# Kernel optimization log

Hardware: AMD Instinct MI355X
Metric: run time of the kernel (lower is better)

The kernel has to match this reference:

```python
import jax, jax.numpy as jnp
import numpy as np

N = 300000   # nodes
E = 1500000  # edges
G = 30000    # graphs
R = 3        # relations
EMB = 32
HID = 64
OUT = 2


def rgcn_conv(x, src, dst, edge_type, W, root, bias, num_nodes):
    """PyG RGCNConv: out_i = x_i @ root + bias + sum_r mean_{j in N_r(i)} x_j @ W_r."""
    out = x @ root + bias
    for r in range(W.shape[0]):
        xr = x @ W[r]                                  # [N, out] transform once per relation
        mask = (edge_type == r).astype(x.dtype)        # [E]
        msg = xr[src] * mask[:, None]                  # gather + mask  [E, out]
        agg = jax.ops.segment_sum(msg, dst, num_segments=num_nodes)
        cnt = jax.ops.segment_sum(mask, dst, num_segments=num_nodes)
        out = out + agg / jnp.maximum(cnt, 1.0)[:, None]
    return out


def global_mean_pool(x, batch, num_graphs):
    s = jax.ops.segment_sum(x, batch, num_segments=num_graphs)
    c = jax.ops.segment_sum(jnp.ones((x.shape[0],), x.dtype), batch, num_segments=num_graphs)
    return s / jnp.maximum(c, 1.0)[:, None]


def setup_inputs() -> dict:
    key = jax.random.key(0)
    ks = jax.random.split(key, 16)
    def glorot(k, shape):
        fan_in, fan_out = shape[-2], shape[-1]
        lim = np.sqrt(6.0 / (fan_in + fan_out)).astype(np.float32)
        return jax.random.uniform(k, shape, jnp.float32, -lim, lim)
    return {
        "sid": jax.random.randint(ks[0], (N,), 0, 26),
        "cid": jax.random.randint(ks[1], (N,), 0, 10),
        "pid": jax.random.randint(ks[2], (N,), 0, 128),
        "edge_index": jax.random.randint(ks[3], (2, E), 0, N),
        "edge_type": jax.random.randint(ks[4], (E,), 0, R),
        "batch": jnp.sort(jax.random.randint(ks[5], (N,), 0, G)),
        "num_graphs": G,
        "shape_emb": jax.random.normal(ks[6], (26, EMB), jnp.float32),
        "col_emb": jax.random.normal(ks[7], (10, EMB), jnp.float32),
        "pos_emb": jax.random.normal(ks[8], (128, EMB), jnp.float32),
        "W1": glorot(ks[9], (R, EMB, HID)),
        "root1": glorot(ks[10], (EMB, HID)),
        "b1": jnp.zeros((HID,), jnp.float32),
        "W2": glorot(ks[11], (R, HID, HID)),
        "root2": glorot(ks[12], (HID, HID)),
        "b2": jnp.zeros((HID,), jnp.float32),
        "lin_W": glorot(ks[13], (HID, OUT)),
        "lin_b": jnp.zeros((OUT,), jnp.float32),
    }


def reference(sid, cid, pid, edge_index, edge_type, batch, num_graphs,
              shape_emb, col_emb, pos_emb,
              W1, root1, b1, W2, root2, b2, lin_W, lin_b):
    num_nodes = sid.shape[0]
    src, dst = edge_index[0], edge_index[1]
    x = shape_emb[sid] + col_emb[cid] + pos_emb[pid]          # [N, 32]
    x = jax.nn.relu(rgcn_conv(x, src, dst, edge_type, W1, root1, b1, num_nodes))
    x = jax.nn.relu(rgcn_conv(x, src, dst, edge_type, W2, root2, b2, num_nodes))
    g = global_mean_pool(x, batch, num_graphs)                 # [G, 64]
    return g @ lin_W + lin_b                                   # [G, 2]
```

## Files before the change

kernel.cpp:

```cpp
#include <hip/hip_runtime.h>
#include <hip/hip_bf16.h>

#define NREL 3
#define EMB 32
#define HID 64
#define OVCAP 1024
#define BCAP 1024

typedef __attribute__((ext_vector_type(8))) short short8_t;
typedef __attribute__((ext_vector_type(4))) short short4_t;
typedef __attribute__((ext_vector_type(4))) float f32x4;

__device__ inline short f2bf(float v) {
  __hip_bfloat16 b = __float2bfloat16(v);
  short s;
  __builtin_memcpy(&s, &b, 2);
  return s;
}
__device__ inline float bf2f(short s) {
  __hip_bfloat16 b;
  __builtin_memcpy(&b, &s, 2);
  return __bfloat162float(b);
}
__device__ inline void split8(const float* v, short8_t* h, short8_t* l) {
#pragma unroll
  for (int i = 0; i < 8; i++) {
    short hh = f2bf(v[i]);
    (*h)[i] = hh;
    (*l)[i] = f2bf(v[i] - bf2f(hh));
  }
}

__global__ __launch_bounds__(256) void prep_k(
    const int* __restrict__ sid, const int* __restrict__ cid, const int* __restrict__ pid,
    const float* __restrict__ se, const float* __restrict__ ce, const float* __restrict__ pe,
    short* __restrict__ xh, short* __restrict__ xl,
    const int* __restrict__ src, const int* __restrict__ dst, const int* __restrict__ et,
    int* __restrict__ bcur, unsigned* __restrict__ pk,
    const float* __restrict__ root1, const float* __restrict__ W1,
    const float* __restrict__ root2, const float* __restrict__ W2,
    short* __restrict__ w1h, short* __restrict__ w1l,
    short* __restrict__ w2h, short* __restrict__ w2l, int N, int E) {
  int i = blockIdx.x * 256 + threadIdx.x;
  if (i < N * 8) {
    int n = i >> 3, cg = i & 7;
    const float4 a = *(const float4*)&se[sid[n] * EMB + cg * 4];
    const float4 b = *(const float4*)&ce[cid[n] * EMB + cg * 4];
    const float4 c = *(const float4*)&pe[pid[n] * EMB + cg * 4];
    float v[4];
    v[0] = a.x + b.x + c.x; v[1] = a.y + b.y + c.y;
    v[2] = a.z + b.z + c.z; v[3] = a.w + b.w + c.w;
    short4_t h, l;
#pragma unroll
    for (int j = 0; j < 4; j++) {
      short hh = f2bf(v[j]);
      h[j] = hh;
      l[j] = f2bf(v[j] - bf2f(hh));
    }
    *(short4_t*)&xh[(size_t)n * EMB + cg * 4] = h;
    *(short4_t*)&xl[(size_t)n * EMB + cg * 4] = l;
  }
  if (i < E) {
    int d = dst[i];
    int b = d >> 6;
    int j = atomicAdd(&bcur[b * 16], 1);
    if (j < BCAP)
      pk[(size_t)b * BCAP + j] =
          ((unsigned)(d & 63) << 21) | ((unsigned)et[i] << 19) | (unsigned)src[i];
  }
  if (i < 64 * 128) {
    int k = i >> 6, n = i & 63;
    float v = (k < EMB) ? root1[k * 64 + n] : W1[(k - EMB) * 64 + n];
    short h = f2bf(v);
    w1h[n * 128 + k] = h;
    w1l[n * 128 + k] = f2bf(v - bf2f(h));
  }
  if (i < 64 * 256) {
    int k = i >> 6, n = i & 63;
    float v = (k < HID) ? root2[k * 64 + n] : W2[(k - HID) * 64 + n];
    short h = f2bf(v);
    w2h[n * 256 + k] = h;
    w2l[n * 256 + k] = f2bf(v - bf2f(h));
  }
}

__global__ __launch_bounds__(256) void l1fused_k(
    const short* __restrict__ xh, const short* __restrict__ xl,
    const int* __restrict__ bcur, const unsigned* __restrict__ pk,
    const short* __restrict__ wth, const short* __restrict__ wtl,
    const float* __restrict__ bias, short* __restrict__ h1h, short* __restrict__ h1l, int N) {
  __shared__ __align__(16) short lws[64][16][8];
  __shared__ __align__(16) int4 mid_s[192];
  __shared__ int cnt_s[192];
  __shared__ unsigned ovf_s[OVCAP];
  __shared__ int ovfn_s;

  const int t = threadIdx.x;
  const int lane = t & 63, w = t >> 6;
  const int m_ = lane & 15, q = lane >> 4;
  const int n0b = blockIdx.x * 64;

  int node_c = n0b + w * 16 + m_;
  if (node_c >= N) node_c = N - 1;
  short8_t ah0 = *(const short8_t*)&xh[(size_t)node_c * EMB + q * 8];
  short8_t al0 = *(const short8_t*)&xl[(size_t)node_c * EMB + q * 8];
#pragma unroll
  for (int i = 0; i < 4; i++) {
    int chi = t + 256 * i;
    int row = chi >> 4, c = chi & 15;
    short8_t wv = *(const short8_t*)&wth[(size_t)row * 128 + c * 8];
    *(short8_t*)&lws[row][c ^ (row & 7)][0] = wv;
  }
  if (t < 192) cnt_s[t] = 0;
  if (t == 0) ovfn_s = 0;
  __syncthreads();

  {
    int ne = bcur[blockIdx.x * 16];
    if (ne > BCAP) ne = BCAP;
    const size_t base = (size_t)blockIdx.x * BCAP;
    for (int e = t; e < ne; e += 256) {
      unsigned p = pk[base + e];
      int srcn = (int)(p & 0x7FFFF);
      int slot = (int)((p >> 19) & 3) * 64 + (int)(p >> 21);
      int j = atomicAdd(&cnt_s[slot], 1);
      if (j < 4) ((int*)&mid_s[slot])[j] = srcn;
      else {
        int k2 = atomicAdd(&ovfn_s, 1);
        if (k2 < OVCAP) ovf_s[k2] = ((unsigned)slot << 19) | (unsigned)srcn;
      }
    }
  }
  __syncthreads();

  short8_t ahv[4], alv[4];
  ahv[0] = ah0;
  alv[0] = al0;
  {
    int ovn = ovfn_s;
    if (ovn > OVCAP) ovn = OVCAP;
    int tslot[3], tlen[3];
    int4 tid4[3];
#pragma unroll
    for (int k = 0; k < 3; k++) {
      tslot[k] = k * 64 + w * 16 + m_;
      tid4[k] = mid_s[tslot[k]];
      tlen[k] = cnt_s[tslot[k]];
    }
    short8_t v0[3], v1[3], v2[3], v3[3];
#pragma unroll
    for (int k = 0; k < 3; k++) {
      int nself = n0b + (tslot[k] & 63);
      if (nself >= N) nself = N - 1;
      int g0 = (0 < tlen[k]) ? tid4[k].x : nself;
      int g1 = (1 < tlen[k]) ? tid4[k].y : nself;
      int g2 = (2 < tlen[k]) ? tid4[k].z : nself;
      int g3 = (3 < tlen[k]) ? tid4[k].w : nself;
      size_t co = (size_t)q * 8;
      v0[k] = *(const short8_t*)&xh[(size_t)g0 * EMB + co];
      v1[k] = *(const short8_t*)&xh[(size_t)g1 * EMB + co];
      v2[k] = *(const short8_t*)&xh[(size_t)g2 * EMB + co];
      v3[k] = *(const short8_t*)&xh[(size_t)g3 * EMB + co];
    }
#pragma unroll
    for (int k = 0; k < 3; k++) {
      float a[8];
      float k0 = (0 < tlen[k]) ? 1.f : 0.f;
      float k1 = (1 < tlen[k]) ? 1.f : 0.f;
      float k2 = (2 < tlen[k]) ? 1.f : 0.f;
      float k3 = (3 < tlen[k]) ? 1.f : 0.f;
#pragma unroll
      for (int i = 0; i < 8; i++)
        a[i] = k0 * bf2f(v0[k][i]) + k1 * bf2f(v1[k][i]) + k2 * bf2f(v2[k][i]) +
               k3 * bf2f(v3[k][i]);
      for (int k3_ = 0; k3_ < ovn; k3_++) {
        unsigned ov = ovf_s[k3_];
        if ((int)(ov >> 19) == tslot[k]) {
          short8_t u = *(const short8_t*)&xh[(size_t)(ov & 0x7FFFF) * EMB + q * 8];
#pragma unroll
          for (int i = 0; i < 8; i++) a[i] += bf2f(u[i]);
        }
      }
      float inv = 1.f / fmaxf((float)tlen[k], 1.f);
#pragma unroll
      for (int i = 0; i < 8; i++) a[i] *= inv;
      split8(a, &ahv[k + 1], &alv[k + 1]);
    }
  }

  f32x4 acc[4];
#pragma unroll
  for (int i = 0; i < 4; i++) acc[i] = (f32x4){0.f, 0.f, 0.f, 0.f};
#pragma unroll
  for (int g = 0; g < 4; g++) {
#pragma unroll
    for (int tt = 0; tt < 4; tt++) {
      int row = 16 * tt + m_;
      int cs = (g * 4 + q) ^ (row & 7);
      short8_t bh = *(const short8_t*)&lws[row][cs][0];
      acc[tt] = __builtin_amdgcn_mfma_f32_16x16x32_bf16(ahv[g], bh, acc[tt], 0, 0, 0);
      acc[tt] = __builtin_amdgcn_mfma_f32_16x16x32_bf16(alv[g], bh, acc[tt], 0, 0, 0);
    }
  }
  __syncthreads();

#pragma unroll
  for (int i = 0; i < 4; i++) {
    int chi = t + 256 * i;
    int row = chi >> 4, c = chi & 15;
    short8_t wv = *(const short8_t*)&wtl[(size_t)row * 128 + c * 8];
    *(short8_t*)&lws[row][c ^ (row & 7)][0] = wv;
  }
  __syncthreads();

#pragma unroll
  for (int g = 0; g < 4; g++) {
#pragma unroll
    for (int tt = 0; tt < 4; tt++) {
      int row = 16 * tt + m_;
      int cs = (g * 4 + q) ^ (row & 7);
      short8_t bl = *(const short8_t*)&lws[row][cs][0];
      acc[tt] = __builtin_amdgcn_mfma_f32_16x16x32_bf16(ahv[g], bl, acc[tt], 0, 0, 0);
    }
  }
#pragma unroll
  for (int tt = 0; tt < 4; tt++) {
    float bia = bias[16 * tt + m_];
#pragma unroll
    for (int reg = 0; reg < 4; reg++) {
      int node = n0b + w * 16 + q * 4 + reg;
      if (node < N) {
        float val = fmaxf(acc[tt][reg] + bia, 0.f);
        short hh = f2bf(val);
        h1h[(size_t)node * HID + 16 * tt + m_] = hh;
        h1l[(size_t)node * HID + 16 * tt + m_] = f2bf(val - bf2f(hh));
      }
    }
  }
}

__global__ __launch_bounds__(256) void l2fused_k(
    const short* __restrict__ h1h, const short* __restrict__ h1l,
    const int* __restrict__ bcur, const unsigned* __restrict__ pk,
    const short* __restrict__ wth, const short* __restrict__ wtl,
    const float* __restrict__ bias, const float* __restrict__ linW,
    const int* __restrict__ batch, float* __restrict__ gs, float* __restrict__ gc, int N) {
  __shared__ __align__(16) short lws[64][16][8];
  __shared__ __align__(16) int4 mid_s[192];
  __shared__ int cnt_s[192];
  __shared__ unsigned ovf_s[OVCAP];
  __shared__ int ovfn_s;

  const int t = threadIdx.x;
  const int lane = t & 63, w = t >> 6;
  const int m_ = lane & 15, q = lane >> 4;
  const int n0b = blockIdx.x * 64;

  int node_c = n0b + w * 16 + m_;
  if (node_c >= N) node_c = N - 1;
#pragma unroll
  for (int i = 0; i < 4; i++) {
    int chi = t + 256 * i;
    int row = chi >> 4, c = chi & 15;
    int g = c >> 2, qq = c & 3;
    short8_t wv = *(const short8_t*)&wth[(size_t)row * 256 + g * 64 + 0 * 32 + qq * 8];
    *(short8_t*)&lws[row][c ^ (row & 7)][0] = wv;
  }
  if (t < 192) cnt_s[t] = 0;
  if (t == 0) ovfn_s = 0;
  __syncthreads();

  {
    int ne = bcur[blockIdx.x * 16];
    if (ne > BCAP) ne = BCAP;
    const size_t base = (size_t)blockIdx.x * BCAP;
    for (int e = t; e < ne; e += 256) {
      unsigned p = pk[base + e];
      int srcn = (int)(p & 0x7FFFF);
      int slot = (int)((p >> 19) & 3) * 64 + (int)(p >> 21);
      int j = atomicAdd(&cnt_s[slot], 1);
      if (j < 4) ((int*)&mid_s[slot])[j] = srcn;
      else {
        int k2 = atomicAdd(&ovfn_s, 1);
        if (k2 < OVCAP) ovf_s[k2] = ((unsigned)slot << 19) | (unsigned)srcn;
      }
    }
  }
  __syncthreads();

  short8_t ahv0[4], alv0[4], ahv1[4], alv1[4];
  {
    ahv0[0] = *(const short8_t*)&h1h[(size_t)node_c * HID + q * 8];
    alv0[0] = *(const short8_t*)&h1l[(size_t)node_c * HID + q * 8];
    ahv1[0] = *(const short8_t*)&h1h[(size_t)node_c * HID + 32 + q * 8];
    alv1[0] = *(const short8_t*)&h1l[(size_t)node_c * HID + 32 + q * 8];
    int ovn = ovfn_s;
    if (ovn > OVCAP) ovn = OVCAP;
    int tslot[3], tlen[3];
    int4 tid4[3];
    int gid[3][4];
#pragma unroll
    for (int k = 0; k < 3; k++) {
      tslot[k] = k * 64 + w * 16 + m_;
      tid4[k] = mid_s[tslot[k]];
      tlen[k] = cnt_s[tslot[k]];
      int nself = n0b + (tslot[k] & 63);
      if (nself >= N) nself = N - 1;
      gid[k][0] = (0 < tlen[k]) ? tid4[k].x : nself;
      gid[k][1] = (1 < tlen[k]) ? tid4[k].y : nself;
      gid[k][2] = (2 < tlen[k]) ? tid4[k].z : nself;
      gid[k][3] = (3 < tlen[k]) ? tid4[k].w : nself;
    }
    float a0[3][8], a1[3][8];
    {
      short8_t v0[3], v1[3], v2[3], v3[3];
#pragma unroll
      for (int k = 0; k < 3; k++) {
        size_t co = (size_t)q * 8;
        v0[k] = *(const short8_t*)&h1h[(size_t)gid[k][0] * HID + co];
        v1[k] = *(const short8_t*)&h1h[(size_t)gid[k][1] * HID + co];
        v2[k] = *(const short8_t*)&h1h[(size_t)gid[k][2] * HID + co];
        v3[k] = *(const short8_t*)&h1h[(size_t)gid[k][3] * HID + co];
      }
#pragma unroll
      for (int k = 0; k < 3; k++) {
        float k0 = (0 < tlen[k]) ? 1.f : 0.f;
        float k1 = (1 < tlen[k]) ? 1.f : 0.f;
        float k2 = (2 < tlen[k]) ? 1.f : 0.f;
        float k3 = (3 < tlen[k]) ? 1.f : 0.f;
#pragma unroll
        for (int i = 0; i < 8; i++)
          a0[k][i] = k0 * bf2f(v0[k][i]) + k1 * bf2f(v1[k][i]) + k2 * bf2f(v2[k][i]) +
                     k3 * bf2f(v3[k][i]);
      }
    }
    {
      short8_t v0[3], v1[3], v2[3], v3[3];
#pragma unroll
      for (int k = 0; k < 3; k++) {
        size_t co = 32 + (size_t)q * 8;
        v0[k] = *(const short8_t*)&h1h[(size_t)gid[k][0] * HID + co];
        v1[k] = *(const short8_t*)&h1h[(size_t)gid[k][1] * HID + co];
        v2[k] = *(const short8_t*)&h1h[(size_t)gid[k][2] * HID + co];
        v3[k] = *(const short8_t*)&h1h[(size_t)gid[k][3] * HID + co];
      }
#pragma unroll
      for (int k = 0; k < 3; k++) {
        float k0 = (0 < tlen[k]) ? 1.f : 0.f;
        float k1 = (1 < tlen[k]) ? 1.f : 0.f;
        float k2 = (2 < tlen[k]) ? 1.f : 0.f;
        float k3 = (3 < tlen[k]) ? 1.f : 0.f;
#pragma unroll
        for (int i = 0; i < 8; i++)
          a1[k][i] = k0 * bf2f(v0[k][i]) + k1 * bf2f(v1[k][i]) + k2 * bf2f(v2[k][i]) +
                     k3 * bf2f(v3[k][i]);
      }
    }
#pragma unroll
    for (int k = 0; k < 3; k++) {
      for (int k3_ = 0; k3_ < ovn; k3_++) {
        unsigned ov = ovf_s[k3_];
        if ((int)(ov >> 19) == tslot[k]) {
          const short* p = &h1h[(size_t)(ov & 0x7FFFF) * HID];
          short8_t u0 = *(const short8_t*)&p[q * 8];
          short8_t u1 = *(const short8_t*)&p[32 + q * 8];
#pragma unroll
          for (int i = 0; i < 8; i++) {
            a0[k][i] += bf2f(u0[i]);
            a1[k][i] += bf2f(u1[i]);
          }
        }
      }
      float inv = 1.f / fmaxf((float)tlen[k], 1.f);
#pragma unroll
      for (int i = 0; i < 8; i++) {
        a0[k][i] *= inv;
        a1[k][i] *= inv;
      }
      split8(a0[k], &ahv0[k + 1], &alv0[k + 1]);
      split8(a1[k], &ahv1[k + 1], &alv1[k + 1]);
    }
  }

  f32x4 acc[4];
#pragma unroll
  for (int i = 0; i < 4; i++) acc[i] = (f32x4){0.f, 0.f, 0.f, 0.f};
#pragma unroll
  for (int s_ = 0; s_ < 2; s_++) {
    if (s_ == 1) {
#pragma unroll
      for (int i = 0; i < 4; i++) {
        int chi = t + 256 * i;
        int row = chi >> 4, c = chi & 15;
        int g = c >> 2, q2 = c & 3;
        short8_t wv = *(const short8_t*)&wth[(size_t)row * 256 + g * 64 + 32 + q2 * 8];
        *(short8_t*)&lws[row][c ^ (row & 7)][0] = wv;
      }
      __syncthreads();
    }
#pragma unroll
    for (int g = 0; g < 4; g++) {
      short8_t ah = (s_ == 0) ? ahv0[g] : ahv1[g];
      short8_t al = (s_ == 0) ? alv0[g] : alv1[g];
#pragma unroll
      for (int tt = 0; tt < 4; tt++) {
        int row = 16 * tt + m_;
        int cs = (g * 4 + q) ^ (row & 7);
        short8_t bh = *(const short8_t*)&lws[row][cs][0];
        acc[tt] = __builtin_amdgcn_mfma_f32_16x16x32_bf16(ah, bh, acc[tt], 0, 0, 0);
        acc[tt] = __builtin_amdgcn_mfma_f32_16x16x32_bf16(al, bh, acc[tt], 0, 0, 0);
      }
    }
    __syncthreads();
#pragma unroll
    for (int i = 0; i < 4; i++) {
      int chi = t + 256 * i;
      int row = chi >> 4, c = chi & 15;
      int g = c >> 2, q2 = c & 3;
      short8_t wv = *(const short8_t*)&wtl[(size_t)row * 256 + g * 64 + s_ * 32 + q2 * 8];
      *(short8_t*)&lws[row][c ^ (row & 7)][0] = wv;
    }
    __syncthreads();
#pragma unroll
    for (int g = 0; g < 4; g++) {
      short8_t ah = (s_ == 0) ? ahv0[g] : ahv1[g];
#pragma unroll
      for (int tt = 0; tt < 4; tt++) {
        int row = 16 * tt + m_;
        int cs = (g * 4 + q) ^ (row & 7);
        short8_t bl = *(const short8_t*)&lws[row][cs][0];
        acc[tt] = __builtin_amdgcn_mfma_f32_16x16x32_bf16(ah, bl, acc[tt], 0, 0, 0);
      }
    }
    if (s_ == 0) __syncthreads();
  }

  float bia[4], lw0[4], lw1[4];
#pragma unroll
  for (int tt = 0; tt < 4; tt++) {
    int col = 16 * tt + m_;
    bia[tt] = bias[col];
    lw0[tt] = linW[col * 2 + 0];
    lw1[tt] = linW[col * 2 + 1];
  }
#pragma unroll
  for (int reg = 0; reg < 4; reg++) {
    int node = n0b + w * 16 + q * 4 + reg;
    float p0 = 0.f, p1 = 0.f;
#pragma unroll
    for (int tt = 0; tt < 4; tt++) {
      float v = fmaxf(acc[tt][reg] + bia[tt], 0.f);
      p0 += v * lw0[tt];
      p1 += v * lw1[tt];
    }
#pragma unroll
    for (int o = 1; o < 16; o <<= 1) {
      p0 += __shfl_xor(p0, o, 64);
      p1 += __shfl_xor(p1, o, 64);
    }
    if (m_ == 0 && node < N) {
      int g = batch[node];
      atomicAdd(&gs[g * 2 + 0], p0);
      atomicAdd(&gs[g * 2 + 1], p1);
      atomicAdd(&gc[g], 1.0f);
    }
  }
}

__global__ __launch_bounds__(256) void final_k(const float* __restrict__ gs,
                                               const float* __restrict__ gc,
                                               const float* __restrict__ linb,
                                               float* __restrict__ out, int G) {
  int i = blockIdx.x * 256 + threadIdx.x;
  if (i >= G * 2) return;
  int g = i >> 1, o = i & 1;
  out[i] = gs[i] / fmaxf(gc[g], 1.0f) + linb[o];
}

extern "C" void kernel_launch(void* const* d_in, const int* in_sizes, int n_in,
                              void* d_out, int out_size, void* d_ws, size_t ws_size,
                              hipStream_t stream) {
  const int* sid = (const int*)d_in[0];
  const int* cid = (const int*)d_in[1];
  const int* pid = (const int*)d_in[2];
  const int* ei = (const int*)d_in[3];
  const int* et = (const int*)d_in[4];
  const int* batch = (const int*)d_in[5];
  const float* se = (const float*)d_in[7];
  const float* ce = (const float*)d_in[8];
  const float* pe = (const float*)d_in[9];
  const float* W1 = (const float*)d_in[10];
  const float* root1 = (const float*)d_in[11];
  const float* b1 = (const float*)d_in[12];
  const float* W2 = (const float*)d_in[13];
  const float* root2 = (const float*)d_in[14];
  const float* b2 = (const float*)d_in[15];
  const float* linW = (const float*)d_in[16];
  const float* linb = (const float*)d_in[17];
  float* out = (float*)d_out;

  const int N = in_sizes[0];
  const int E = in_sizes[4];
  const int G = out_size / 2;
  const int* src = ei;
  const int* dst = ei + E;
  const int NBk = (N + 63) / 64;
  const int NBa = (NBk + 15) & ~15;

  char* w = (char*)d_ws;
  short* h1h = (short*)w;  w += (size_t)N * HID * sizeof(short);
  short* h1l = (short*)w;  w += (size_t)N * HID * sizeof(short);
  short* xh = (short*)w;   w += (size_t)N * EMB * sizeof(short);
  short* xl = (short*)w;   w += (size_t)N * EMB * sizeof(short);
  float* gs = (float*)w;   w += (size_t)G * 2 * sizeof(float);
  float* gc = (float*)w;   w += (size_t)G * sizeof(float);
  int* bcur = (int*)w;     w += (size_t)NBa * 16 * sizeof(int);
  unsigned* pk = (unsigned*)w; w += (size_t)NBa * BCAP * sizeof(unsigned);
  short* w1h = (short*)w;  w += (size_t)64 * 128 * sizeof(short);
  short* w1l = (short*)w;  w += (size_t)64 * 128 * sizeof(short);
  short* w2h = (short*)w;  w += (size_t)64 * 256 * sizeof(short);
  short* w2l = (short*)w;  w += (size_t)64 * 256 * sizeof(short);
  if ((size_t)(w - (char*)d_ws) > ws_size) return;

  hipMemsetAsync(bcur, 0, (size_t)NBa * 16 * sizeof(int), stream);
  hipMemsetAsync(gs, 0, (size_t)G * 3 * sizeof(float), stream);

  int prep_n = N * 8;
  if (prep_n < E) prep_n = E;
  if (prep_n < 64 * 256) prep_n = 64 * 256;
  prep_k<<<(prep_n + 255) / 256, 256, 0, stream>>>(sid, cid, pid, se, ce, pe, xh, xl, src,
                                                   dst, et, bcur, pk, root1, W1, root2, W2,
                                                   w1h, w1l, w2h, w2l, N, E);

  l1fused_k<<<NBk, 256, 0, stream>>>(xh, xl, bcur, pk, w1h, w1l, b1, h1h, h1l, N);
  l2fused_k<<<NBk, 256, 0, stream>>>(h1h, h1l, bcur, pk, w2h, w2l, b2, linW, batch, gs, gc,
                                     N);
  final_k<<<(G * 2 + 255) / 256, 256, 0, stream>>>(gs, gc, linb, out, G);
}
```

Measured before the change: 379.6 us.

## Reuse layer-1 per-block neighbor buckets in layer 2 and merge memsets

Layer 1 already sorts each block's edges into per-slot neighbor lists and overflow lists in shared memory. It now writes these lists back into that block's own segment of the packed-edge buffer. Layer 2 then reads the compact slot lists straight from global memory instead of re-bucketing the edges with shared-memory atomics. The two memsets are also merged into one by placing bcur next to the graph accumulators. In exchange, overflow storage is capped at 63 entries per block, so blocks with many high-degree slots would silently drop edges.

Result: slower. 420.8 us (+10.9%).

```diff
diff --git a/kernel.cpp b/kernel.cpp
--- a/kernel.cpp
+++ b/kernel.cpp
@@ -5,6 +5,7 @@
 #define EMB 32
 #define HID 64
 #define OVCAP 1024
+#define OVDUMP 63
 #define BCAP 1024
 
 typedef __attribute__((ext_vector_type(8))) short short8_t;
@@ -86,7 +87,7 @@
 
 __global__ __launch_bounds__(256) void l1fused_k(
     const short* __restrict__ xh, const short* __restrict__ xl,
-    const int* __restrict__ bcur, const unsigned* __restrict__ pk,
+    const int* __restrict__ bcur, unsigned* __restrict__ pk,
     const short* __restrict__ wth, const short* __restrict__ wtl,
     const float* __restrict__ bias, short* __restrict__ h1h, short* __restrict__ h1l, int N) {
   __shared__ __align__(16) short lws[64][16][8];
@@ -133,6 +134,18 @@
   }
   __syncthreads();
 
+  {
+    unsigned* seg = &pk[(size_t)blockIdx.x * BCAP];
+    if (t < 192) {
+      *(int4*)&seg[t * 4] = mid_s[t];
+      seg[768 + t] = (unsigned)cnt_s[t];
+    }
+    int ovn = ovfn_s;
+    if (ovn > OVDUMP) ovn = OVDUMP;
+    if (t == 0) seg[960] = (unsigned)ovn;
+    for (int i = t; i < ovn; i += 256) seg[961 + i] = ovf_s[i];
+  }
+
   short8_t ahv[4], alv[4];
   ahv[0] = ah0;
   alv[0] = al0;
@@ -241,20 +254,18 @@
 
 __global__ __launch_bounds__(256) void l2fused_k(
     const short* __restrict__ h1h, const short* __restrict__ h1l,
-    const int* __restrict__ bcur, const unsigned* __restrict__ pk,
+    const unsigned* __restrict__ pk,
     const short* __restrict__ wth, const short* __restrict__ wtl,
     const float* __restrict__ bias, const float* __restrict__ linW,
     const int* __restrict__ batch, float* __restrict__ gs, float* __restrict__ gc, int N) {
   __shared__ __align__(16) short lws[64][16][8];
-  __shared__ __align__(16) int4 mid_s[192];
-  __shared__ int cnt_s[192];
-  __shared__ unsigned ovf_s[OVCAP];
-  __shared__ int ovfn_s;
+  __shared__ unsigned ovf_s[OVDUMP + 1];
 
   const int t = threadIdx.x;
   const int lane = t & 63, w = t >> 6;
   const int m_ = lane & 15, q = lane >> 4;
   const int n0b = blockIdx.x * 64;
+  const unsigned* seg = &pk[(size_t)blockIdx.x * BCAP];
 
   int node_c = n0b + w * 16 + m_;
   if (node_c >= N) node_c = N - 1;
@@ -266,26 +277,9 @@
     short8_t wv = *(const short8_t*)&wth[(size_t)row * 256 + g * 64 + 0 * 32 + qq * 8];
     *(short8_t*)&lws[row][c ^ (row & 7)][0] = wv;
   }
-  if (t < 192) cnt_s[t] = 0;
-  if (t == 0) ovfn_s = 0;
-  __syncthreads();
-
-  {
-    int ne = bcur[blockIdx.x * 16];
-    if (ne > BCAP) ne = BCAP;
-    const size_t base = (size_t)blockIdx.x * BCAP;
-    for (int e = t; e < ne; e += 256) {
-      unsigned p = pk[base + e];
-      int srcn = (int)(p & 0x7FFFF);
-      int slot = (int)((p >> 19) & 3) * 64 + (int)(p >> 21);
-      int j = atomicAdd(&cnt_s[slot], 1);
-      if (j < 4) ((int*)&mid_s[slot])[j] = srcn;
-      else {
-        int k2 = atomicAdd(&ovfn_s, 1);
-        if (k2 < OVCAP) ovf_s[k2] = ((unsigned)slot << 19) | (unsigned)srcn;
-      }
-    }
-  }
+  int ovn = (int)seg[960];
+  if (ovn > OVDUMP) ovn = OVDUMP;
+  for (int i = t; i < ovn; i += 256) ovf_s[i] = seg[961 + i];
   __syncthreads();
 
   short8_t ahv0[4], alv0[4], ahv1[4], alv1[4];
@@ -294,16 +288,14 @@
     alv0[0] = *(const short8_t*)&h1l[(size_t)node_c * HID + q * 8];
     ahv1[0] = *(const short8_t*)&h1h[(size_t)node_c * HID + 32 + q * 8];
     alv1[0] = *(const short8_t*)&h1l[(size_t)node_c * HID + 32 + q * 8];
-    int ovn = ovfn_s;
-    if (ovn > OVCAP) ovn = OVCAP;
     int tslot[3], tlen[3];
     int4 tid4[3];
     int gid[3][4];
 #pragma unroll
     for (int k = 0; k < 3; k++) {
       tslot[k] = k * 64 + w * 16 + m_;
-      tid4[k] = mid_s[tslot[k]];
-      tlen[k] = cnt_s[tslot[k]];
+      tid4[k] = *(const int4*)&seg[tslot[k] * 4];
+      tlen[k] = (int)seg[768 + tslot[k]];
       int nself = n0b + (tslot[k] & 63);
       if (nself >= N) nself = N - 1;
       gid[k][0] = (0 < tlen[k]) ? tid4[k].x : nself;
@@ -512,9 +504,9 @@
   short* h1l = (short*)w;  w += (size_t)N * HID * sizeof(short);
   short* xh = (short*)w;   w += (size_t)N * EMB * sizeof(short);
   short* xl = (short*)w;   w += (size_t)N * EMB * sizeof(short);
+  int* bcur = (int*)w;     w += (size_t)NBa * 16 * sizeof(int);
   float* gs = (float*)w;   w += (size_t)G * 2 * sizeof(float);
   float* gc = (float*)w;   w += (size_t)G * sizeof(float);
-  int* bcur = (int*)w;     w += (size_t)NBa * 16 * sizeof(int);
   unsigned* pk = (unsigned*)w; w += (size_t)NBa * BCAP * sizeof(unsigned);
   short* w1h = (short*)w;  w += (size_t)64 * 128 * sizeof(short);
   short* w1l = (short*)w;  w += (size_t)64 * 128 * sizeof(short);
@@ -522,8 +514,8 @@
   short* w2l = (short*)w;  w += (size_t)64 * 256 * sizeof(short);
   if ((size_t)(w - (char*)d_ws) > ws_size) return;
 
-  hipMemsetAsync(bcur, 0, (size_t)NBa * 16 * sizeof(int), stream);
-  hipMemsetAsync(gs, 0, (size_t)G * 3 * sizeof(float), stream);
+  hipMemsetAsync(bcur, 0, (size_t)NBa * 16 * sizeof(int) + (size_t)G * 3 * sizeof(float),
+                 stream);
 
   int prep_n = N * 8;
   if (prep_n < E) prep_n = E;
@@ -533,7 +525,6 @@
                                                    w1h, w1l, w2h, w2l, N, E);
 
   l1fused_k<<<NBk, 256, 0, stream>>>(xh, xl, bcur, pk, w1h, w1l, b1, h1h, h1l, N);
-  l2fused_k<<<NBk, 256, 0, stream>>>(h1h, h1l, bcur, pk, w2h, w2l, b2, linW, batch, gs, gc,
-                                     N);
+  l2fused_k<<<NBk, 256, 0, stream>>>(h1h, h1l, pk, w2h, w2l, b2, linW, batch, gs, gc, N);
   final_k<<<(G * 2 + 255) / 256, 256, 0, stream>>>(gs, gc, linb, out, G);
 }
```
